# Kernel optimization log

Hardware: AMD Instinct MI355X
Metric: run time of the kernel (lower is better)

## Reference

```python
import jax, jax.numpy as jnp
import numpy as np

_BLOCK = 32          # _QUANTIZATION_BLOCK_SIZE
_UPPER = 8           # upper_bound = 2**(4-1)-1 + 1 for Q4_0 (bitwidth=4)
_QMAX = 15.0         # 2**bitwidth - 1


def _q4_0_dequant(kernel):
    """Vectorized Q4_0 fake-quantization over 32-element blocks (last axis, no transpose)."""
    orig_dtype = kernel.dtype
    nb = kernel.size // _BLOCK
    blocks = kernel.reshape(nb, _BLOCK).astype(jnp.float32)  # [nb, 32]
    # signed value at the abs-argmax position of each block
    amax_idx = jnp.argmax(jnp.abs(blocks), axis=1)
    max_val = jnp.take_along_axis(blocks, amax_idx[:, None], axis=1)  # [nb, 1]
    d = -max_val / _UPPER
    safe_d = jnp.where(d == 0.0, 1.0, d)
    safe_inv_d = jnp.where(d == 0.0, 0.0, 1.0 / safe_d)
    scale = d.astype(jnp.float16).astype(jnp.float32)  # fp16 scale round-trip
    qs = jnp.clip(jnp.trunc(blocks * safe_inv_d + (_UPPER + 0.5)), 0.0, _QMAX)
    deq = scale * (qs - _UPPER)
    return deq.reshape(kernel.shape).astype(orig_dtype)


def _ste_q4_0(kernel):
    """Straight-through estimator wrapper (identity gradient)."""
    zero = kernel - jax.lax.stop_gradient(kernel)
    return zero + jax.lax.stop_gradient(_q4_0_dequant(kernel))


def setup_inputs() -> dict:
    key = jax.random.key(0)
    k1, k2, k3 = jax.random.split(key, 3)
    d_in, features = 8192, 8192
    inputs = jax.random.normal(k1, (1, 32, d_in), dtype=jnp.float32)
    kernel = jax.random.normal(k2, (d_in, features), dtype=jnp.float32) * 0.02
    bias = jax.random.normal(k3, (features,), dtype=jnp.float32) * 0.02
    return {"inputs": inputs, "kernel": kernel, "bias": bias}


def reference(inputs, kernel, bias):
    w = _ste_q4_0(kernel)                      # fake-quantized weight [d_in, features]
    y = inputs @ w                             # [B, S, features]
    y = y + bias
    return y
```

## Files before the change

### kernel.cpp

```cpp
#include <hip/hip_runtime.h>
#include <hip/hip_fp16.h>

#define MDIM 32
#define KDIM 8192
#define NDIM 8192
#define NT 128
#define KC 512
#define BK 64
#define NTILES (KC / BK)
#define WPAD 132

typedef _Float16 half2_t __attribute__((ext_vector_type(2)));

#if __has_builtin(__builtin_amdgcn_fdot2)
__device__ __forceinline__ float fdot2(half2_t a, half2_t b, float c) {
  return __builtin_amdgcn_fdot2(a, b, c, false);
}
#else
__device__ __forceinline__ float fdot2(half2_t a, half2_t b, float c) {
  return c + (float)a.x * (float)b.x + (float)a.y * (float)b.y;
}
#endif

__device__ __forceinline__ unsigned pk_u32(float a, float b) {
#if __has_builtin(__builtin_amdgcn_cvt_pkrtz)
  return __builtin_bit_cast(unsigned, __builtin_amdgcn_cvt_pkrtz(a, b));
#else
  half2_t r; r.x = (_Float16)a; r.y = (_Float16)b;
  return __builtin_bit_cast(unsigned, r);
#endif
}

__device__ __forceinline__ half2_t u2h(unsigned u) {
  return __builtin_bit_cast(half2_t, u);
}

__global__ __launch_bounds__(256) void xpack_kernel(const float* __restrict__ x,
                                                    unsigned* __restrict__ xp) {
  __shared__ float sx[32][129];
  const int t  = threadIdx.x;
  const int k0 = blockIdx.x * 128;
  {
    const int m = t >> 3, c = (t & 7) * 16;
    const float* p = x + (size_t)m * KDIM + k0 + c;
#pragma unroll
    for (int j = 0; j < 4; ++j) {
      float4 v = reinterpret_cast<const float4*>(p)[j];
      sx[m][c + j * 4 + 0] = v.x;
      sx[m][c + j * 4 + 1] = v.y;
      sx[m][c + j * 4 + 2] = v.z;
      sx[m][c + j * 4 + 3] = v.w;
    }
  }
  __syncthreads();
  const int kpl = t & 63, mh = t >> 6;
  unsigned pw[8];
#pragma unroll
  for (int j = 0; j < 8; ++j) {
    int mm = mh * 8 + j;
    pw[j] = pk_u32(sx[mm][2 * kpl], sx[mm][2 * kpl + 1]);
  }
  uint4* dst = reinterpret_cast<uint4*>(xp + ((size_t)(k0 >> 1) + kpl) * 32 + mh * 8);
  dst[0] = make_uint4(pw[0], pw[1], pw[2], pw[3]);
  dst[1] = make_uint4(pw[4], pw[5], pw[6], pw[7]);
}

__global__ __launch_bounds__(256, 4) void fused_q4_gemm(
    const float* __restrict__ x,
    const unsigned* __restrict__ xp,
    const float* __restrict__ w,
    const float* __restrict__ bias,
    float* __restrict__ out)
{
  __shared__ unsigned s_w2[32 * WPAD];

  const int t  = threadIdx.x;
  const int n0 = blockIdx.x * NT;
  const int k0 = blockIdx.y * KC;

  const int kr = t >> 3;
  const int nc = t & 7;
  const int n_local = t & 127;
  const int gn = n0 + n_local;
  const int mbase = (__builtin_amdgcn_readfirstlane(t) >> 7) << 4;

  float acc[16];
#pragma unroll
  for (int j = 0; j < 16; ++j) acc[j] = 0.0f;

  for (int tt = 0; tt < NTILES; ++tt) {
    const int kt = k0 + tt * BK;

    {
      const float* rp = w + (size_t)(kt + 2 * kr) * NDIM + n0 + nc * 16;
      float4 v0[4], v1[4];
#pragma unroll
      for (int j = 0; j < 4; ++j) {
        v0[j] = reinterpret_cast<const float4*>(rp)[j];
        v1[j] = reinterpret_cast<const float4*>(rp + NDIM)[j];
      }
      float ba0 = -1.0f, bv0 = 0.0f, ba1 = -1.0f, bv1 = 0.0f;
#pragma unroll
      for (int j = 0; j < 4; ++j) {
        float c, a;
        c = v0[j].x; a = fabsf(c); if (a > ba0) { ba0 = a; bv0 = c; }
        c = v0[j].y; a = fabsf(c); if (a > ba0) { ba0 = a; bv0 = c; }
        c = v0[j].z; a = fabsf(c); if (a > ba0) { ba0 = a; bv0 = c; }
        c = v0[j].w; a = fabsf(c); if (a > ba0) { ba0 = a; bv0 = c; }
        c = v1[j].x; a = fabsf(c); if (a > ba1) { ba1 = a; bv1 = c; }
        c = v1[j].y; a = fabsf(c); if (a > ba1) { ba1 = a; bv1 = c; }
        c = v1[j].z; a = fabsf(c); if (a > ba1) { ba1 = a; bv1 = c; }
        c = v1[j].w; a = fabsf(c); if (a > ba1) { ba1 = a; bv1 = c; }
      }
      float pa0 = __shfl_xor(ba0, 1), pv0 = __shfl_xor(bv0, 1);
      float pa1 = __shfl_xor(ba1, 1), pv1 = __shfl_xor(bv1, 1);
      const bool odd = (t & 1);
      if (odd ? (pa0 >= ba0) : (pa0 > ba0)) bv0 = pv0;
      if (odd ? (pa1 >= ba1) : (pa1 > ba1)) bv1 = pv1;

      float d0 = bv0 * -0.125f;
      float i0 = (d0 == 0.0f) ? 0.0f : 1.0f / d0;
      float s0 = __half2float(__float2half(d0));
      float d1 = bv1 * -0.125f;
      float i1 = (d1 == 0.0f) ? 0.0f : 1.0f / d1;
      float s1 = __half2float(__float2half(d1));

      unsigned pw[16];
#pragma unroll
      for (int j = 0; j < 4; ++j) {
        float q, a0f, a1f;
#define DQ(comp, idx)                                                      \
        q = fminf(fmaxf(truncf(fmaf(v0[j].comp, i0, 8.5f)), 0.0f), 15.0f); \
        a0f = (q - 8.0f) * s0;                                             \
        q = fminf(fmaxf(truncf(fmaf(v1[j].comp, i1, 8.5f)), 0.0f), 15.0f); \
        a1f = (q - 8.0f) * s1;                                             \
        pw[j * 4 + idx] = pk_u32(a0f, a1f);
        DQ(x, 0) DQ(y, 1) DQ(z, 2) DQ(w, 3)
#undef DQ
      }
      uint4* wp = reinterpret_cast<uint4*>(&s_w2[kr * WPAD + nc * 16]);
      wp[0] = make_uint4(pw[0],  pw[1],  pw[2],  pw[3]);
      wp[1] = make_uint4(pw[4],  pw[5],  pw[6],  pw[7]);
      wp[2] = make_uint4(pw[8],  pw[9],  pw[10], pw[11]);
      wp[3] = make_uint4(pw[12], pw[13], pw[14], pw[15]);
    }

    __syncthreads();

    const int kb = kt >> 1;
#pragma unroll 4
    for (int kp = 0; kp < BK / 2; ++kp) {
      half2_t w2 = u2h(s_w2[kp * WPAD + n_local]);
      const uint4* xr = reinterpret_cast<const uint4*>(xp + (size_t)(kb + kp) * 32 + mbase);
      uint4 q0 = xr[0], q1 = xr[1], q2 = xr[2], q3 = xr[3];
      acc[0]  = fdot2(w2, u2h(q0.x), acc[0]);
      acc[1]  = fdot2(w2, u2h(q0.y), acc[1]);
      acc[2]  = fdot2(w2, u2h(q0.z), acc[2]);
      acc[3]  = fdot2(w2, u2h(q0.w), acc[3]);
      acc[4]  = fdot2(w2, u2h(q1.x), acc[4]);
      acc[5]  = fdot2(w2, u2h(q1.y), acc[5]);
      acc[6]  = fdot2(w2, u2h(q1.z), acc[6]);
      acc[7]  = fdot2(w2, u2h(q1.w), acc[7]);
      acc[8]  = fdot2(w2, u2h(q2.x), acc[8]);
      acc[9]  = fdot2(w2, u2h(q2.y), acc[9]);
      acc[10] = fdot2(w2, u2h(q2.z), acc[10]);
      acc[11] = fdot2(w2, u2h(q2.w), acc[11]);
      acc[12] = fdot2(w2, u2h(q3.x), acc[12]);
      acc[13] = fdot2(w2, u2h(q3.y), acc[13]);
      acc[14] = fdot2(w2, u2h(q3.z), acc[14]);
      acc[15] = fdot2(w2, u2h(q3.w), acc[15]);
    }
    __syncthreads();
  }

  const float bv = (blockIdx.y == 0) ? bias[gn] : 0.0f;
#pragma unroll
  for (int j = 0; j < 16; ++j) {
    atomicAdd(out + (size_t)(mbase + j) * NDIM + gn, acc[j] + bv);
  }
}

extern "C" void kernel_launch(void* const* d_in, const int* in_sizes, int n_in,
                              void* d_out, int out_size, void* d_ws, size_t ws_size,
                              hipStream_t stream) {
  const float* x    = (const float*)d_in[0];
  const float* w    = (const float*)d_in[1];
  const float* bias = (const float*)d_in[2];
  float* out  = (float*)d_out;
  unsigned* xp = (unsigned*)d_ws;

  (void)hipMemsetAsync(out, 0, (size_t)MDIM * NDIM * sizeof(float), stream);
  xpack_kernel<<<64, 256, 0, stream>>>(x, xp);

  dim3 grid(NDIM / NT, KDIM / KC);
  fused_q4_gemm<<<grid, 256, 0, stream>>>(x, xp, w, bias, out);
}
```

Before: 372.4 us.

## Replace fdot2 inner product with MFMA 16x16x32 f16 and fragment-packed activations

Swaps the per-thread fdot2 accumulation loop for MFMA 16x16x32 f16 matrix instructions. Each wave computes a 32x32 output tile. Activations are pre-packed into the MFMA A-fragment layout by a simpler xpack kernel. The dequantized weights are stored transposed in LDS (n-major, stride 72) so B fragments load as 16-byte vectors. The goal is to cut the VALU cost of the dot-product phase, at the price of scattered 4-byte LDS stores during dequant and a changed atomic epilogue layout.

After: 373.4 us. No clear change (+0.3%).

```diff
diff --git a/kernel.cpp b/kernel.cpp
--- a/kernel.cpp
+++ b/kernel.cpp
@@ -8,71 +8,46 @@
 #define KC 512
 #define BK 64
 #define NTILES (KC / BK)
-#define WPAD 132
+#define WSTRIDE 72
 
-typedef _Float16 half2_t __attribute__((ext_vector_type(2)));
-
-#if __has_builtin(__builtin_amdgcn_fdot2)
-__device__ __forceinline__ float fdot2(half2_t a, half2_t b, float c) {
-  return __builtin_amdgcn_fdot2(a, b, c, false);
-}
-#else
-__device__ __forceinline__ float fdot2(half2_t a, half2_t b, float c) {
-  return c + (float)a.x * (float)b.x + (float)a.y * (float)b.y;
-}
-#endif
+typedef __fp16 half8 __attribute__((ext_vector_type(8)));
+typedef float f32x4 __attribute__((ext_vector_type(4)));
 
 __device__ __forceinline__ unsigned pk_u32(float a, float b) {
 #if __has_builtin(__builtin_amdgcn_cvt_pkrtz)
   return __builtin_bit_cast(unsigned, __builtin_amdgcn_cvt_pkrtz(a, b));
 #else
-  half2_t r; r.x = (_Float16)a; r.y = (_Float16)b;
-  return __builtin_bit_cast(unsigned, r);
+  __fp16 r2[2] = {(__fp16)a, (__fp16)b};
+  return __builtin_bit_cast(unsigned, r2);
 #endif
 }
 
-__device__ __forceinline__ half2_t u2h(unsigned u) {
-  return __builtin_bit_cast(half2_t, u);
-}
-
 __global__ __launch_bounds__(256) void xpack_kernel(const float* __restrict__ x,
-                                                    unsigned* __restrict__ xp) {
-  __shared__ float sx[32][129];
-  const int t  = threadIdx.x;
-  const int k0 = blockIdx.x * 128;
-  {
-    const int m = t >> 3, c = (t & 7) * 16;
-    const float* p = x + (size_t)m * KDIM + k0 + c;
-#pragma unroll
-    for (int j = 0; j < 4; ++j) {
-      float4 v = reinterpret_cast<const float4*>(p)[j];
-      sx[m][c + j * 4 + 0] = v.x;
-      sx[m][c + j * 4 + 1] = v.y;
-      sx[m][c + j * 4 + 2] = v.z;
-      sx[m][c + j * 4 + 3] = v.w;
-    }
-  }
-  __syncthreads();
-  const int kpl = t & 63, mh = t >> 6;
-  unsigned pw[8];
-#pragma unroll
-  for (int j = 0; j < 8; ++j) {
-    int mm = mh * 8 + j;
-    pw[j] = pk_u32(sx[mm][2 * kpl], sx[mm][2 * kpl + 1]);
-  }
-  uint4* dst = reinterpret_cast<uint4*>(xp + ((size_t)(k0 >> 1) + kpl) * 32 + mh * 8);
-  dst[0] = make_uint4(pw[0], pw[1], pw[2], pw[3]);
-  dst[1] = make_uint4(pw[4], pw[5], pw[6], pw[7]);
+                                                    uint4* __restrict__ xpf) {
+  const int T  = blockIdx.x * 256 + threadIdx.x;
+  const int sg = T >> 7;
+  const int r  = T & 127;
+  const int mt = r >> 6;
+  const int L  = r & 63;
+  const int m  = mt * 16 + (L & 15);
+  const int k  = sg * 32 + (L >> 4) * 8;
+  const float4* p = reinterpret_cast<const float4*>(x + (size_t)m * KDIM + k);
+  float4 u0 = p[0], u1 = p[1];
+  uint4 o;
+  o.x = pk_u32(u0.x, u0.y);
+  o.y = pk_u32(u0.z, u0.w);
+  o.z = pk_u32(u1.x, u1.y);
+  o.w = pk_u32(u1.z, u1.w);
+  xpf[T] = o;
 }
 
 __global__ __launch_bounds__(256, 4) void fused_q4_gemm(
-    const float* __restrict__ x,
-    const unsigned* __restrict__ xp,
+    const uint4* __restrict__ xpf,
     const float* __restrict__ w,
     const float* __restrict__ bias,
     float* __restrict__ out)
 {
-  __shared__ unsigned s_w2[32 * WPAD];
+  __shared__ _Float16 s_w[NT * WSTRIDE];
 
   const int t  = threadIdx.x;
   const int n0 = blockIdx.x * NT;
@@ -80,13 +55,18 @@
 
   const int kr = t >> 3;
   const int nc = t & 7;
-  const int n_local = t & 127;
-  const int gn = n0 + n_local;
-  const int mbase = (__builtin_amdgcn_readfirstlane(t) >> 7) << 4;
 
-  float acc[16];
-#pragma unroll
-  for (int j = 0; j < 16; ++j) acc[j] = 0.0f;
+  const int lane = t & 63;
+  const int wv   = t >> 6;
+  const int l15  = lane & 15;
+  const int q    = lane >> 4;
+
+  f32x4 acc00 = {0.f, 0.f, 0.f, 0.f};
+  f32x4 acc01 = {0.f, 0.f, 0.f, 0.f};
+  f32x4 acc10 = {0.f, 0.f, 0.f, 0.f};
+  f32x4 acc11 = {0.f, 0.f, 0.f, 0.f};
+
+  unsigned* sw32 = reinterpret_cast<unsigned*>(s_w);
 
   for (int tt = 0; tt < NTILES; ++tt) {
     const int kt = k0 + tt * BK;
@@ -128,55 +108,58 @@
       unsigned pw[16];
 #pragma unroll
       for (int j = 0; j < 4; ++j) {
-        float q, a0f, a1f;
-#define DQ(comp, idx)                                                      \
-        q = fminf(fmaxf(truncf(fmaf(v0[j].comp, i0, 8.5f)), 0.0f), 15.0f); \
-        a0f = (q - 8.0f) * s0;                                             \
-        q = fminf(fmaxf(truncf(fmaf(v1[j].comp, i1, 8.5f)), 0.0f), 15.0f); \
-        a1f = (q - 8.0f) * s1;                                             \
+        float qv, a0f, a1f;
+#define DQ(comp, idx)                                                        \
+        qv = fminf(fmaxf(truncf(fmaf(v0[j].comp, i0, 8.5f)), 0.0f), 15.0f);  \
+        a0f = (qv - 8.0f) * s0;                                              \
+        qv = fminf(fmaxf(truncf(fmaf(v1[j].comp, i1, 8.5f)), 0.0f), 15.0f);  \
+        a1f = (qv - 8.0f) * s1;                                              \
         pw[j * 4 + idx] = pk_u32(a0f, a1f);
         DQ(x, 0) DQ(y, 1) DQ(z, 2) DQ(w, 3)
 #undef DQ
       }
-      uint4* wp = reinterpret_cast<uint4*>(&s_w2[kr * WPAD + nc * 16]);
-      wp[0] = make_uint4(pw[0],  pw[1],  pw[2],  pw[3]);
-      wp[1] = make_uint4(pw[4],  pw[5],  pw[6],  pw[7]);
-      wp[2] = make_uint4(pw[8],  pw[9],  pw[10], pw[11]);
-      wp[3] = make_uint4(pw[12], pw[13], pw[14], pw[15]);
+#pragma unroll
+      for (int i = 0; i < 16; ++i) {
+        const int n = nc * 16 + i;
+        sw32[n * (WSTRIDE / 2) + kr] = pw[i];
+      }
     }
 
     __syncthreads();
 
-    const int kb = kt >> 1;
-#pragma unroll 4
-    for (int kp = 0; kp < BK / 2; ++kp) {
-      half2_t w2 = u2h(s_w2[kp * WPAD + n_local]);
-      const uint4* xr = reinterpret_cast<const uint4*>(xp + (size_t)(kb + kp) * 32 + mbase);
-      uint4 q0 = xr[0], q1 = xr[1], q2 = xr[2], q3 = xr[3];
-      acc[0]  = fdot2(w2, u2h(q0.x), acc[0]);
-      acc[1]  = fdot2(w2, u2h(q0.y), acc[1]);
-      acc[2]  = fdot2(w2, u2h(q0.z), acc[2]);
-      acc[3]  = fdot2(w2, u2h(q0.w), acc[3]);
-      acc[4]  = fdot2(w2, u2h(q1.x), acc[4]);
-      acc[5]  = fdot2(w2, u2h(q1.y), acc[5]);
-      acc[6]  = fdot2(w2, u2h(q1.z), acc[6]);
-      acc[7]  = fdot2(w2, u2h(q1.w), acc[7]);
-      acc[8]  = fdot2(w2, u2h(q2.x), acc[8]);
-      acc[9]  = fdot2(w2, u2h(q2.y), acc[9]);
-      acc[10] = fdot2(w2, u2h(q2.z), acc[10]);
-      acc[11] = fdot2(w2, u2h(q2.w), acc[11]);
-      acc[12] = fdot2(w2, u2h(q3.x), acc[12]);
-      acc[13] = fdot2(w2, u2h(q3.y), acc[13]);
-      acc[14] = fdot2(w2, u2h(q3.z), acc[14]);
-      acc[15] = fdot2(w2, u2h(q3.w), acc[15]);
+    const int sgbase = kt >> 5;
+#pragma unroll
+    for (int ks = 0; ks < 2; ++ks) {
+      const uint4* ap = xpf + ((size_t)(sgbase + ks) * 2) * 64 + lane;
+      uint4 a0u = ap[0];
+      uint4 a1u = ap[64];
+      const int kl = ks * 32 + q * 8;
+      uint4 b0u = *reinterpret_cast<const uint4*>(&s_w[(wv * 32 + l15) * WSTRIDE + kl]);
+      uint4 b1u = *reinterpret_cast<const uint4*>(&s_w[(wv * 32 + 16 + l15) * WSTRIDE + kl]);
+      half8 a0 = __builtin_bit_cast(half8, a0u);
+      half8 a1 = __builtin_bit_cast(half8, a1u);
+      half8 b0 = __builtin_bit_cast(half8, b0u);
+      half8 b1 = __builtin_bit_cast(half8, b1u);
+      acc00 = __builtin_amdgcn_mfma_f32_16x16x32_f16(a0, b0, acc00, 0, 0, 0);
+      acc01 = __builtin_amdgcn_mfma_f32_16x16x32_f16(a0, b1, acc01, 0, 0, 0);
+      acc10 = __builtin_amdgcn_mfma_f32_16x16x32_f16(a1, b0, acc10, 0, 0, 0);
+      acc11 = __builtin_amdgcn_mfma_f32_16x16x32_f16(a1, b1, acc11, 0, 0, 0);
     }
     __syncthreads();
   }
 
-  const float bv = (blockIdx.y == 0) ? bias[gn] : 0.0f;
+  const int gn0 = n0 + wv * 32 + l15;
+  const int gn1 = gn0 + 16;
+  const float bv0 = (blockIdx.y == 0) ? bias[gn0] : 0.0f;
+  const float bv1 = (blockIdx.y == 0) ? bias[gn1] : 0.0f;
 #pragma unroll
-  for (int j = 0; j < 16; ++j) {
-    atomicAdd(out + (size_t)(mbase + j) * NDIM + gn, acc[j] + bv);
+  for (int r = 0; r < 4; ++r) {
+    const int m0 = q * 4 + r;
+    const int m1 = 16 + q * 4 + r;
+    atomicAdd(out + (size_t)m0 * NDIM + gn0, acc00[r] + bv0);
+    atomicAdd(out + (size_t)m0 * NDIM + gn1, acc01[r] + bv1);
+    atomicAdd(out + (size_t)m1 * NDIM + gn0, acc10[r] + bv0);
+    atomicAdd(out + (size_t)m1 * NDIM + gn1, acc11[r] + bv1);
   }
 }
 
@@ -187,11 +170,11 @@
   const float* w    = (const float*)d_in[1];
   const float* bias = (const float*)d_in[2];
   float* out  = (float*)d_out;
-  unsigned* xp = (unsigned*)d_ws;
+  uint4* xpf  = (uint4*)d_ws;
 
   (void)hipMemsetAsync(out, 0, (size_t)MDIM * NDIM * sizeof(float), stream);
-  xpack_kernel<<<64, 256, 0, stream>>>(x, xp);
+  xpack_kernel<<<128, 256, 0, stream>>>(x, xpf);
 
   dim3 grid(NDIM / NT, KDIM / KC);
-  fused_q4_gemm<<<grid, 256, 0, stream>>>(x, xp, w, bias, out);
+  fused_q4_gemm<<<grid, 256, 0, stream>>>(xpf, w, bias, out);
 }
```
